# Kernel tuning notes

Hardware: AMD Instinct MI355X
Metric: run time of the kernel (lower is better)

The kernel has to match this reference:

```python
import jax, jax.numpy as jnp
import numpy as np

HEADS = 8
DIM_HEAD = 64
SCALE = DIM_HEAD ** -0.5
LN_EPS = 1e-5
NEG_INF = -1e30


def layernorm(x, gamma, beta):
    mu = jnp.mean(x, axis=-1, keepdims=True)
    var = jnp.var(x, axis=-1, keepdims=True)
    return (x - mu) * jax.lax.rsqrt(var + LN_EPS) * gamma + beta


def setup_inputs() -> dict:
    key = jax.random.key(0)
    ks = jax.random.split(key, 8)
    b, f, n, d, inner = 8, 8192, 64, 1024, HEADS * DIM_HEAD
    x = jax.random.normal(ks[0], (b, f, d), dtype=jnp.float32)
    latents = jax.random.normal(ks[1], (b, n, d), dtype=jnp.float32)
    key_padding_mask = jax.random.randint(ks[2], (b, f), 0, 2) > 0  # True = padded
    s = 0.02
    return {
        "x": x,
        "latents": latents,
        "key_padding_mask": key_padding_mask,
        "kv_gate": jnp.float32(-4.0),
        "gamma_media": jnp.ones((d,), jnp.float32),
        "beta_media": jnp.zeros((d,), jnp.float32),
        "gamma_lat": jnp.ones((d,), jnp.float32),
        "beta_lat": jnp.zeros((d,), jnp.float32),
        "Wq": jax.random.normal(ks[3], (d, inner), jnp.float32) * s,
        "Wk": jax.random.normal(ks[4], (d, inner), jnp.float32) * s,
        "Wv": jax.random.normal(ks[5], (d, inner), jnp.float32) * s,
        "Wout": jax.random.normal(ks[6], (inner, d), jnp.float32) * s,
    }


def reference(x, latents, key_padding_mask, kv_gate, gamma_media, beta_media,
              gamma_lat, beta_lat, Wq, Wk, Wv, Wout):
    b, f, d = x.shape
    n = latents.shape[1]
    x = layernorm(x, gamma_media, beta_media)
    latents = layernorm(latents, gamma_lat, beta_lat)
    kv = jnp.concatenate((x, latents * kv_gate), axis=1)  # (b, f+n, d)

    q = (latents @ Wq).reshape(b, n, HEADS, DIM_HEAD)       # (b, q, h, d)
    k = (kv @ Wk).reshape(b, f + n, HEADS, DIM_HEAD)        # (b, kv, h, d)
    v = (kv @ Wv).reshape(b, f + n, HEADS, DIM_HEAD)

    sim = jnp.einsum('bqhd,bkhd->bhqk', q * SCALE, k)       # (b, h, n, f+n)
    sim = sim - jax.lax.stop_gradient(jnp.max(sim, axis=-1, keepdims=True))

    valid_feat = ~key_padding_mask                          # (b, f)
    valid_full = jnp.concatenate(
        (valid_feat, jnp.ones((b, n), dtype=bool)), axis=1)  # (b, f+n)
    sim = jnp.where(valid_full[:, None, None, :], sim, NEG_INF)

    attn = jax.nn.softmax(sim, axis=-1)
    out = jnp.einsum('bhqk,bkhd->bqhd', attn, v).reshape(b, n, HEADS * DIM_HEAD)
    return out @ Wout
```

## Files before the change

### kernel.cpp

```cpp
#include <hip/hip_runtime.h>
#include <stdint.h>


#define KVPAD 8448
#define NCHUNK 17

typedef __attribute__((ext_vector_type(8))) short short8;
typedef __attribute__((ext_vector_type(4))) float f32x4;

typedef __attribute__((address_space(1))) void gvoid;
typedef __attribute__((address_space(3))) void lvoid;

__device__ __forceinline__ unsigned short f2bf(float f) {
    union { float f; uint32_t u; } v; v.f = f;
    uint32_t u = v.u;
    u += 0x7fffu + ((u >> 16) & 1u);
    return (unsigned short)(u >> 16);
}

__device__ __forceinline__ void mfma16(f32x4& c, short8 a, short8 b) {
    asm volatile("v_mfma_f32_16x16x32_bf16 %0, %1, %2, %0"
                 : "+v"(c) : "v"(a), "v"(b));
}

__device__ __forceinline__ void gl2lds16(const void* g, void* l) {
    __builtin_amdgcn_global_load_lds((gvoid*)g, (lvoid*)l, 16, 0, 0);
}

__device__ __forceinline__ void pbar() {
    asm volatile("" ::: "memory");
    __builtin_amdgcn_s_barrier();
    asm volatile("" ::: "memory");
}
#define WAITVM(N) asm volatile("s_waitcnt vmcnt(" #N ")" ::: "memory")

__global__ __launch_bounds__(1024) void scan_kernel(
    const int* __restrict__ mask, int* __restrict__ pfx, int* __restrict__ cnt)
{
    __shared__ int wsum[16];
    int b = blockIdx.x;
    int t = threadIdx.x, lane = t & 63, w = t >> 6;
    int c[8], tot = 0;
#pragma unroll
    for (int k = 0; k < 8; k++) {
        c[k] = (mask[b * 8192 + k * 1024 + t] == 0) ? 1 : 0;
        tot += c[k];
    }
    int run = tot;
#pragma unroll
    for (int off = 1; off < 64; off <<= 1) {
        int u = __shfl_up(run, off);
        if (lane >= off) run += u;
    }
    if (lane == 63) wsum[w] = run;
    __syncthreads();
    if (t < 16) {
        int v = wsum[t];
#pragma unroll
        for (int off = 1; off < 16; off <<= 1) {
            int u = __shfl_up(v, off);
            if (t >= off) v += u;
        }
        wsum[t] = v;
        if (t == 15) cnt[b] = v;
    }
    __syncthreads();
    int base = (w ? wsum[w - 1] : 0) + (run - tot);
#pragma unroll
    for (int k = 0; k < 8; k++) {
        pfx[b * 8192 + k * 1024 + t] = base;
        base += c[k];
    }
}

__global__ __launch_bounds__(256) void prep_kernel(
    const float* __restrict__ X, const float* __restrict__ latents,
    const int* __restrict__ mask, const int* __restrict__ pfx,
    const float* __restrict__ gm, const float* __restrict__ bm,
    const float* __restrict__ gl, const float* __restrict__ bl,
    const float* __restrict__ Wk, const float* __restrict__ Wv,
    const float* __restrict__ Wq, const float* __restrict__ Wout,
    unsigned short* __restrict__ x_ln, unsigned short* __restrict__ lat_ln,
    unsigned short* __restrict__ WkvqT, unsigned short* __restrict__ WoutT)
{
    __shared__ float t[64][65];
    int blk = blockIdx.x;
    if (blk >= 16512) {
        int tt = blk - 16512;
        int z = tt >> 7, u = tt & 127;
        const float* S; unsigned short* D; int R, C, bx, by;
        if (z == 0)      { S = Wk;   D = WkvqT;                       R = 1024; C = 512;  by = u >> 3; bx = u & 7; }
        else if (z == 1) { S = Wv;   D = WkvqT + (size_t)512 * 1024;  R = 1024; C = 512;  by = u >> 3; bx = u & 7; }
        else if (z == 2) { S = Wq;   D = WkvqT + (size_t)1024 * 1024; R = 1024; C = 512;  by = u >> 3; bx = u & 7; }
        else             { S = Wout; D = WoutT;                       R = 512;  C = 1024; by = u >> 4; bx = u & 15; }
        int r0 = by * 64, c0 = bx * 64;
#pragma unroll
        for (int i = 0; i < 16; i++) {
            int o = i * 256 + threadIdx.x;
            int rr = o >> 6, cc = o & 63;
            t[rr][cc] = S[(size_t)(r0 + rr) * C + c0 + cc];
        }
        __syncthreads();
#pragma unroll
        for (int i = 0; i < 16; i++) {
            int o = i * 256 + threadIdx.x;
            int cl = o >> 6, rl = o & 63;
            D[(size_t)(c0 + cl) * R + r0 + rl] = f2bf(t[rl][cl]);
        }
        return;
    }
    int lane = threadIdx.x & 63;
    int row = blk * 4 + (threadIdx.x >> 6);
    const float *src, *g, *bet;
    unsigned short* dst;
    if (row < 65536) {
        if (mask[row] != 0) return;
        int b = row >> 13;
        src = X + (size_t)row * 1024;
        dst = x_ln + ((size_t)b * 8192 + pfx[row]) * 1024;
        g = gm; bet = bm;
    } else {
        int r = row - 65536;
        src = latents + (size_t)r * 1024;
        dst = lat_ln + (size_t)r * 1024;
        g = gl; bet = bl;
    }
    const float4* xr = (const float4*)src;
    float4 v[4];
    float s = 0.f, s2 = 0.f;
#pragma unroll
    for (int i = 0; i < 4; i++) {
        v[i] = xr[i * 64 + lane];
        s  += v[i].x + v[i].y + v[i].z + v[i].w;
        s2 += v[i].x*v[i].x + v[i].y*v[i].y + v[i].z*v[i].z + v[i].w*v[i].w;
    }
#pragma unroll
    for (int off = 1; off < 64; off <<= 1) {
        s += __shfl_xor(s, off);
        s2 += __shfl_xor(s2, off);
    }
    float mean = s * (1.0f / 1024.0f);
    float var  = s2 * (1.0f / 1024.0f) - mean * mean;
    float rs = rsqrtf(var + 1e-5f);
    ushort4* yr = (ushort4*)dst;
    const float4* gp = (const float4*)g;
    const float4* bp = (const float4*)bet;
#pragma unroll
    for (int i = 0; i < 4; i++) {
        int c4 = i * 64 + lane;
        float4 gg = gp[c4], bb = bp[c4];
        ushort4 o;
        o.x = f2bf((v[i].x - mean) * rs * gg.x + bb.x);
        o.y = f2bf((v[i].y - mean) * rs * gg.y + bb.y);
        o.z = f2bf((v[i].z - mean) * rs * gg.z + bb.z);
        o.w = f2bf((v[i].w - mean) * rs * gg.w + bb.w);
        yr[c4] = o;
    }
}

__global__ __launch_bounds__(512, 2) void gemm256(
    const unsigned short* __restrict__ A,
    const unsigned short* __restrict__ BT,
    unsigned short* __restrict__ Ck,
    unsigned short* __restrict__ CvT,
    const int* __restrict__ cnt)
{
    __shared__ unsigned short lds[65536];
    int bx = blockIdx.x, by = blockIdx.y;
    int lid = by * 4 + bx;
    lid = (lid & 7) * 128 + (lid >> 3);
    bx = lid & 3; by = lid >> 2;
    int rowbase = by * 256;
    int colbase = bx * 256;
    int bq = by >> 5;
    int rl0 = (by & 31) * 256;
    if (rl0 >= cnt[bq]) return;

    int tid = threadIdx.x;
    int lane = tid & 63;
    int wid = tid >> 6;
    int qd = lane >> 4, cc = lane & 15;
    int wm = wid >> 2, wn = wid & 3;

    f32x4 acc[8][4];
#pragma unroll
    for (int mf = 0; mf < 8; mf++)
#pragma unroll
        for (int nf = 0; nf < 4; nf++)
            acc[mf][nf] = (f32x4){0.f, 0.f, 0.f, 0.f};

#define STAGE_TILE(buf, kt)                                                     \
    {                                                                           \
        int bb = (buf) * 32768;                                                 \
        _Pragma("unroll")                                                       \
        for (int i = 0; i < 4; i++) {                                           \
            int s = i * 512 + tid;                                              \
            int m = s >> 3, kc = s & 7;                                         \
            int kg = kc ^ (m & 7);                                              \
            gl2lds16(A + (size_t)(rowbase + m) * 1024 + (kt) * 64 + kg * 8,     \
                     &lds[bb + s * 8]);                                         \
        }                                                                       \
        _Pragma("unroll")                                                       \
        for (int i = 0; i < 4; i++) {                                           \
            int s = i * 512 + tid;                                              \
            int m = s >> 3, kc = s & 7;                                         \
            int kg = kc ^ (m & 7);                                              \
            gl2lds16(BT + (size_t)(colbase + m) * 1024 + (kt) * 64 + kg * 8,    \
                     &lds[bb + 16384 + s * 8]);                                 \
        }                                                                       \
    }

    STAGE_TILE(0, 0);
    WAITVM(0);
    pbar();

    int cur = 0;
#pragma unroll 1
    for (int kt = 0; kt < 16; kt++) {
        bool pf = (kt < 15);
        int ab = cur * 32768;
        int bb = ab + 16384;
        short8 bf0[4], bf1[4], af[4];

        if (pf) STAGE_TILE(cur ^ 1, kt + 1);
#pragma unroll
        for (int nf = 0; nf < 4; nf++) {
            int n = wn * 64 + nf * 16 + cc;
            bf0[nf] = *(const short8*)&lds[bb + (n * 8 + (qd ^ (n & 7))) * 8];
        }
#pragma unroll
        for (int i = 0; i < 4; i++) {
            int m = wm * 128 + i * 16 + cc;
            af[i] = *(const short8*)&lds[ab + (m * 8 + (qd ^ (m & 7))) * 8];
        }
        __builtin_amdgcn_s_setprio(1);
#pragma unroll
        for (int i = 0; i < 4; i++)
#pragma unroll
            for (int nf = 0; nf < 4; nf++)
                mfma16(acc[i][nf], af[i], bf0[nf]);
        __builtin_amdgcn_s_setprio(0);
        pbar();

#pragma unroll
        for (int i = 0; i < 4; i++) {
            int m = wm * 128 + (4 + i) * 16 + cc;
            af[i] = *(const short8*)&lds[ab + (m * 8 + (qd ^ (m & 7))) * 8];
        }
        __builtin_amdgcn_s_setprio(1);
#pragma unroll
        for (int i = 0; i < 4; i++)
#pragma unroll
            for (int nf = 0; nf < 4; nf++)
                mfma16(acc[4 + i][nf], af[i], bf0[nf]);
        __builtin_amdgcn_s_setprio(0);
        pbar();

#pragma unroll
        for (int nf = 0; nf < 4; nf++) {
            int n = wn * 64 + nf * 16 + cc;
            bf1[nf] = *(const short8*)&lds[bb + (n * 8 + ((4 + qd) ^ (n & 7))) * 8];
        }
#pragma unroll
        for (int i = 0; i < 4; i++) {
            int m = wm * 128 + i * 16 + cc;
            af[i] = *(const short8*)&lds[ab + (m * 8 + ((4 + qd) ^ (m & 7))) * 8];
        }
        __builtin_amdgcn_s_setprio(1);
#pragma unroll
        for (int i = 0; i < 4; i++)
#pragma unroll
            for (int nf = 0; nf < 4; nf++)
                mfma16(acc[i][nf], af[i], bf1[nf]);
        __builtin_amdgcn_s_setprio(0);
        pbar();

#pragma unroll
        for (int i = 0; i < 4; i++) {
            int m = wm * 128 + (4 + i) * 16 + cc;
            af[i] = *(const short8*)&lds[ab + (m * 8 + ((4 + qd) ^ (m & 7))) * 8];
        }
        __builtin_amdgcn_s_setprio(1);
#pragma unroll
        for (int i = 0; i < 4; i++)
#pragma unroll
            for (int nf = 0; nf < 4; nf++)
                mfma16(acc[4 + i][nf], af[i], bf1[nf]);
        __builtin_amdgcn_s_setprio(0);
        if (pf) WAITVM(0);
        pbar();
        cur ^= 1;
    }
#undef STAGE_TILE

    bool isK = (colbase < 512);
#pragma unroll
    for (int mf = 0; mf < 8; mf++) {
        int grow = rl0 + wm * 128 + mf * 16 + qd * 4;
#pragma unroll
        for (int nf = 0; nf < 4; nf++) {
            int col = colbase + wn * 64 + nf * 16 + cc;
            if (isK) {
#pragma unroll
                for (int r = 0; r < 4; r++)
                    Ck[(size_t)(bq * KVPAD + 64 + grow + r) * 512 + col] =
                        f2bf(acc[mf][nf][r]);
            } else {
                ushort4 pk;
                pk.x = f2bf(acc[mf][nf][0]);
                pk.y = f2bf(acc[mf][nf][1]);
                pk.z = f2bf(acc[mf][nf][2]);
                pk.w = f2bf(acc[mf][nf][3]);
                *(ushort4*)&CvT[((size_t)bq * 512 + (col - 512)) * KVPAD + 64 + grow] = pk;
            }
        }
    }
}

__global__ __launch_bounds__(256) void gemm_bf16(
    const unsigned short* __restrict__ A, const unsigned short* __restrict__ BT,
    int Kd,
    unsigned short* __restrict__ Ck, float* __restrict__ Cf,
    unsigned short* __restrict__ CvT, unsigned short* __restrict__ Qb,
    int nsplit, int nq, int ldc, int P, int Sstride, int Ofs,
    float scale_const, float qscale, const float* __restrict__ scale_ptr,
    const int* __restrict__ cnt)
{
    __shared__ unsigned short a_lds[128 * 64];
    __shared__ unsigned short b_lds[128 * 64];
    int bx = blockIdx.x, by = blockIdx.y;
    size_t rowbase = (size_t)by * 128;
    size_t colbase = (size_t)bx * 128;
    if (cnt) {
        int bq = (int)rowbase / P, rl = (int)rowbase - bq * P;
        if (rl >= cnt[bq]) return;
    }
    int tid = threadIdx.x;
    int lane = tid & 63;
    int wave = tid >> 6;
    int wrow = (wave >> 1) * 64, wcol = (wave & 1) * 64;
    int qd = lane >> 4, cc = lane & 15;

    f32x4 acc[4][4];
#pragma unroll
    for (int mt = 0; mt < 4; mt++)
#pragma unroll
        for (int nt = 0; nt < 4; nt++)
            acc[mt][nt] = (f32x4){0.f, 0.f, 0.f, 0.f};

    int kiters = Kd >> 6;
    for (int kt = 0; kt < kiters; kt++) {
        int k0 = kt << 6;
#pragma unroll
        for (int i = 0; i < 4; i++) {
            int s = i * 256 + tid;
            int m = s >> 3, kc = s & 7;
            int kg = kc ^ (m & 7);
            gl2lds16(A + (rowbase + m) * (size_t)Kd + (k0 + kg * 8), &a_lds[s * 8]);
        }
#pragma unroll
        for (int i = 0; i < 4; i++) {
            int s = i * 256 + tid;
            int m = s >> 3, kc = s & 7;
            int kg = kc ^ (m & 7);
            gl2lds16(BT + (colbase + m) * (size_t)Kd + (k0 + kg * 8), &b_lds[s * 8]);
        }
        __syncthreads();
#pragma unroll
        for (int ks = 0; ks < 2; ks++) {
            short8 af[4], bfr[4];
            int cg = ks * 4 + qd;
#pragma unroll
            for (int mt = 0; mt < 4; mt++) {
                int m = wrow + mt * 16 + cc;
                af[mt] = *(const short8*)&a_lds[(m * 8 + (cg ^ (m & 7))) * 8];
            }
#pragma unroll
            for (int nt = 0; nt < 4; nt++) {
                int n = wcol + nt * 16 + cc;
                bfr[nt] = *(const short8*)&b_lds[(n * 8 + (cg ^ (n & 7))) * 8];
            }
#pragma unroll
            for (int mt = 0; mt < 4; mt++)
#pragma unroll
                for (int nt = 0; nt < 4; nt++)
                    mfma16(acc[mt][nt], af[mt], bfr[nt]);
        }
        __syncthreads();
    }

    float sc = scale_const;
    if (scale_ptr) sc *= *scale_ptr;
#pragma unroll
    for (int mt = 0; mt < 4; mt++) {
        int g0 = (int)rowbase + wrow + mt * 16 + qd * 4;
        int bq = g0 / P, rl = g0 - bq * P;
#pragma unroll
        for (int nt = 0; nt < 4; nt++) {
            int col = (int)colbase + wcol + nt * 16 + cc;
            if (col >= nq) {
#pragma unroll
                for (int r = 0; r < 4; r++)
                    Qb[(size_t)(bq * 64 + rl + r) * 512 + (col - nq)] =
                        f2bf(acc[mt][nt][r] * qscale);
            } else if (col < nsplit) {
                int idx0 = bq * Sstride + Ofs + rl;
                if (Cf) {
#pragma unroll
                    for (int r = 0; r < 4; r++)
                        Cf[(size_t)(idx0 + r) * ldc + col] = acc[mt][nt][r] * sc;
                } else {
#pragma unroll
                    for (int r = 0; r < 4; r++)
                        Ck[(size_t)(idx0 + r) * ldc + col] = f2bf(acc[mt][nt][r] * sc);
                }
            } else {
                ushort4 pk;
                pk.x = f2bf(acc[mt][nt][0] * sc);
                pk.y = f2bf(acc[mt][nt][1] * sc);
                pk.z = f2bf(acc[mt][nt][2] * sc);
                pk.w = f2bf(acc[mt][nt][3] * sc);
                *(ushort4*)&CvT[((size_t)bq * 512 + (col - nsplit)) * KVPAD + Ofs + rl] = pk;
            }
        }
    }
}

__global__ __launch_bounds__(256) void attn_kernel(
    const unsigned short* __restrict__ Kbuf,
    const unsigned short* __restrict__ Vt,
    const unsigned short* __restrict__ Qbuf,
    const int* __restrict__ cnt,
    float* __restrict__ Opart,
    float* __restrict__ Mpart,
    float* __restrict__ Lpart)
{
    __shared__ unsigned short P_lds[64 * 264];
    __shared__ float red_max[4][64];
    __shared__ float red_sum[4][64];
    __shared__ float mrow[64];
    __shared__ float lrow[64];
    __shared__ float frow[64];

    int chunk = blockIdx.x, h = blockIdx.y, b = blockIdx.z;
    int len = 64 + cnt[b];
    int kv0 = chunk * 512;
    if (kv0 >= len) return;

    int tid = threadIdx.x, lane = tid & 63, w = tid >> 6;
    int qd = lane >> 4, cc = lane & 15;
    int pidx = (b * 8 + h) * NCHUNK + chunk;

    short8 qf[4][2];
    const unsigned short* Qb = Qbuf + ((size_t)b * 64) * 512 + h * 64;
#pragma unroll
    for (int mt = 0; mt < 4; mt++)
#pragma unroll
        for (int ks = 0; ks < 2; ks++)
            qf[mt][ks] = *(const short8*)&Qb[(size_t)(mt * 16 + cc) * 512 + ks * 32 + qd * 8];

    f32x4 acco[4];
#pragma unroll
    for (int mt = 0; mt < 4; mt++) acco[mt] = (f32x4){0.f, 0.f, 0.f, 0.f};

    const unsigned short* Kb = Kbuf + (size_t)b * KVPAD * 512 + h * 64;
    const unsigned short* Vbase = Vt + ((size_t)b * 512 + h * 64 + w * 16 + cc) * KVPAD;

#pragma unroll 1
    for (int s = 0; s < 2; s++) {
        int kvs = kv0 + s * 256;
        if (kvs >= len) break;
        int kvw = kvs + w * 64;

        f32x4 acc[4][4];
#pragma unroll
        for (int mt = 0; mt < 4; mt++)
#pragma unroll
            for (int nt = 0; nt < 4; nt++)
                acc[mt][nt] = (f32x4){0.f, 0.f, 0.f, 0.f};
#pragma unroll
        for (int nt = 0; nt < 4; nt++) {
            int kvr = kvw + nt * 16 + cc;
#pragma unroll
            for (int ks = 0; ks < 2; ks++) {
                short8 kf = *(const short8*)&Kb[(size_t)kvr * 512 + ks * 32 + qd * 8];
#pragma unroll
                for (int mt = 0; mt < 4; mt++)
                    mfma16(acc[mt][nt], qf[mt][ks], kf);
            }
        }
#pragma unroll
        for (int nt = 0; nt < 4; nt++) {
            int kv = kvw + nt * 16 + cc;
            if (kv >= len) {
#pragma unroll
                for (int mt = 0; mt < 4; mt++)
#pragma unroll
                    for (int r = 0; r < 4; r++) acc[mt][nt][r] = -1e30f;
            }
        }
        float vmax[4][4];
#pragma unroll
        for (int mt = 0; mt < 4; mt++)
#pragma unroll
            for (int r = 0; r < 4; r++)
                vmax[mt][r] = fmaxf(fmaxf(acc[mt][0][r], acc[mt][1][r]),
                                    fmaxf(acc[mt][2][r], acc[mt][3][r]));
#pragma unroll
        for (int off = 1; off < 16; off <<= 1)
#pragma unroll
            for (int mt = 0; mt < 4; mt++)
#pragma unroll
                for (int r = 0; r < 4; r++)
                    vmax[mt][r] = fmaxf(vmax[mt][r], __shfl_xor(vmax[mt][r], off));
        if (cc == 0) {
#pragma unroll
            for (int mt = 0; mt < 4; mt++)
#pragma unroll
                for (int r = 0; r < 4; r++)
                    red_max[w][mt * 16 + qd * 4 + r] = vmax[mt][r];
        }
        __syncthreads();
        if (tid < 64) {
            float tmax = fmaxf(fmaxf(red_max[0][tid], red_max[1][tid]),
                               fmaxf(red_max[2][tid], red_max[3][tid]));
            if (s == 0) {
                mrow[tid] = tmax;
            } else {
                float mo = mrow[tid];
                float mn = fmaxf(mo, tmax);
                frow[tid] = __expf(mo - mn);
                mrow[tid] = mn;
            }
        }
        __syncthreads();
        float vsum[4][4];
#pragma unroll
        for (int mt = 0; mt < 4; mt++)
#pragma unroll
            for (int r = 0; r < 4; r++) {
                int row = mt * 16 + qd * 4 + r;
                float m = mrow[row];
                float ssum = 0.f;
#pragma unroll
                for (int nt = 0; nt < 4; nt++) {
                    float p = __expf(acc[mt][nt][r] - m);
                    ssum += p;
                    P_lds[row * 264 + w * 64 + nt * 16 + cc] = f2bf(p);
                }
                vsum[mt][r] = ssum;
            }
#pragma unroll
        for (int off = 1; off < 16; off <<= 1)
#pragma unroll
            for (int mt = 0; mt < 4; mt++)
#pragma unroll
                for (int r = 0; r < 4; r++)
                    vsum[mt][r] += __shfl_xor(vsum[mt][r], off);
        if (cc == 0) {
#pragma unroll
            for (int mt = 0; mt < 4; mt++)
#pragma unroll
                for (int r = 0; r < 4; r++)
                    red_sum[w][mt * 16 + qd * 4 + r] = vsum[mt][r];
        }
        __syncthreads();
        if (tid < 64) {
            float snew = red_sum[0][tid] + red_sum[1][tid] +
                         red_sum[2][tid] + red_sum[3][tid];
            lrow[tid] = (s == 0) ? snew : lrow[tid] * frow[tid] + snew;
        }
        if (s > 0) {
#pragma unroll
            for (int mt = 0; mt < 4; mt++)
#pragma unroll
                for (int r = 0; r < 4; r++)
                    acco[mt][r] *= frow[mt * 16 + qd * 4 + r];
        }
        const unsigned short* Vb = Vbase + kvs;
#pragma unroll
        for (int ks = 0; ks < 8; ks++) {
            short8 vf = *(const short8*)&Vb[ks * 32 + qd * 8];
#pragma unroll
            for (int mt = 0; mt < 4; mt++) {
                short8 pf = *(const short8*)&P_lds[(size_t)(mt * 16 + cc) * 264 + ks * 32 + qd * 8];
                mfma16(acco[mt], pf, vf);
            }
        }
    }

    if (tid < 64) {
        Mpart[(size_t)pidx * 64 + tid] = mrow[tid];
        Lpart[(size_t)pidx * 64 + tid] = lrow[tid];
    }
    float* Ob = Opart + (size_t)pidx * 4096;
#pragma unroll
    for (int mt = 0; mt < 4; mt++)
#pragma unroll
        for (int r = 0; r < 4; r++)
            Ob[(size_t)(mt * 16 + qd * 4 + r) * 64 + w * 16 + cc] = acco[mt][r];
}

__global__ __launch_bounds__(256) void combine_kernel(
    const float* __restrict__ Opart, const float* __restrict__ Mpart,
    const float* __restrict__ Lpart, const int* __restrict__ cnt,
    unsigned short* __restrict__ AttnOut)
{
    __shared__ float wls[NCHUNK][16];
    __shared__ float invl[16];
    int bh = blockIdx.x >> 2, qg = blockIdx.x & 3;
    int b = bh >> 3, h = bh & 7;
    int pbase = bh * NCHUNK;
    int nact = (64 + cnt[b] + 511) >> 9;
    int tid = threadIdx.x;
    if (tid < 16) {
        int q = qg * 16 + tid;
        float M = -3.0e38f;
        for (int cn = 0; cn < nact; cn++)
            M = fmaxf(M, Mpart[(size_t)(pbase + cn) * 64 + q]);
        float l = 0.f;
        for (int cn = 0; cn < nact; cn++) {
            float wc = __expf(Mpart[(size_t)(pbase + cn) * 64 + q] - M);
            wls[cn][tid] = wc;
            l += wc * Lpart[(size_t)(pbase + cn) * 64 + q];
        }
        invl[tid] = 1.0f / l;
    }
    __syncthreads();
    int ql = tid >> 4, d4 = (tid & 15) * 4;
    int q = qg * 16 + ql;
    float ax = 0.f, ay = 0.f, az = 0.f, aw = 0.f;
    for (int cn = 0; cn < nact; cn++) {
        float wc = wls[cn][ql];
        float4 o = *(const float4*)&Opart[((size_t)(pbase + cn) * 64 + q) * 64 + d4];
        ax += wc * o.x; ay += wc * o.y; az += wc * o.z; aw += wc * o.w;
    }
    float iv = invl[ql];
    ushort4 pk;
    pk.x = f2bf(ax * iv); pk.y = f2bf(ay * iv);
    pk.z = f2bf(az * iv); pk.w = f2bf(aw * iv);
    *(ushort4*)&AttnOut[((size_t)b * 64 + q) * 512 + h * 64 + d4] = pk;
}

#define OPART_OFF    ((size_t)0)
#define MPART_OFF    ((size_t)34603008)
#define LPART_OFF    ((size_t)35143680)
#define XLN_OFF      ((size_t)0)
#define LATLN_OFF    ((size_t)134217728)
#define KBUF_OFF     ((size_t)135266304)
#define VT_OFF       ((size_t)204472320)
#define WKVQT_OFF    ((size_t)273678336)
#define WOUTT_OFF    ((size_t)276824064)
#define PFX_OFF      ((size_t)277872640)
#define CNT_OFF      ((size_t)278134784)
#define QBUF_OFF     ((size_t)278134912)
#define ATTNOUT_OFF  ((size_t)278659200)

extern "C" void kernel_launch(void* const* d_in, const int* in_sizes, int n_in,
                              void* d_out, int out_size, void* d_ws, size_t ws_size,
                              hipStream_t stream) {
    const float* x       = (const float*)d_in[0];
    const float* latents = (const float*)d_in[1];
    const int*   mask    = (const int*)d_in[2];
    const float* kv_gate = (const float*)d_in[3];
    const float* gm      = (const float*)d_in[4];
    const float* bm      = (const float*)d_in[5];
    const float* gl      = (const float*)d_in[6];
    const float* bl      = (const float*)d_in[7];
    const float* Wq      = (const float*)d_in[8];
    const float* Wk      = (const float*)d_in[9];
    const float* Wv      = (const float*)d_in[10];
    const float* Wout    = (const float*)d_in[11];
    float* out = (float*)d_out;

    char* ws = (char*)d_ws;
    float* Opart = (float*)(ws + OPART_OFF);
    float* Mpart = (float*)(ws + MPART_OFF);
    float* Lpart = (float*)(ws + LPART_OFF);
    unsigned short* Qbuf    = (unsigned short*)(ws + QBUF_OFF);
    unsigned short* AttnOut = (unsigned short*)(ws + ATTNOUT_OFF);
    unsigned short* x_ln    = (unsigned short*)(ws + XLN_OFF);
    unsigned short* lat_ln  = (unsigned short*)(ws + LATLN_OFF);
    unsigned short* Kbuf    = (unsigned short*)(ws + KBUF_OFF);
    unsigned short* Vt      = (unsigned short*)(ws + VT_OFF);
    unsigned short* WkvqT   = (unsigned short*)(ws + WKVQT_OFF);
    unsigned short* WoutT   = (unsigned short*)(ws + WOUTT_OFF);
    int* pfx = (int*)(ws + PFX_OFF);
    int* cnt = (int*)(ws + CNT_OFF);

    scan_kernel<<<8, 1024, 0, stream>>>(mask, pfx, cnt);

    prep_kernel<<<17024, 256, 0, stream>>>(
        x, latents, mask, pfx, gm, bm, gl, bl, Wk, Wv, Wq, Wout,
        x_ln, lat_ln, WkvqT, WoutT);

    gemm_bf16<<<dim3(12, 4), 256, 0, stream>>>(
        lat_ln, WkvqT, 1024, Kbuf, nullptr, Vt, Qbuf,
        512, 1024, 512, 64, KVPAD, 0, 1.0f, 0.125f, kv_gate, nullptr);

    gemm256<<<dim3(4, 256), 512, 0, stream>>>(x_ln, WkvqT, Kbuf, Vt, cnt);

    attn_kernel<<<dim3(NCHUNK, 8, 8), 256, 0, stream>>>(
        Kbuf, Vt, Qbuf, cnt, Opart, Mpart, Lpart);

    combine_kernel<<<256, 256, 0, stream>>>(Opart, Mpart, Lpart, cnt, AttnOut);

    gemm_bf16<<<dim3(8, 4), 256, 0, stream>>>(
        AttnOut, WoutT, 512, nullptr, out, nullptr, nullptr,
        1 << 30, 1 << 30, 1024, 64, 64, 0, 1.0f, 0.f, nullptr, nullptr);
}
```

Measured before the change: 539.3 us.

## Interleave half-tile global-to-LDS staging with MFMA phases in KV projection GEMM

Restructures the K/V projection GEMM main loop into a finer-grained software pipeline. Tiles are now staged in half-tile pieces, interleaved between MFMA sub-blocks, and B tiles are prefetched one step further ahead, with partial vmcnt waits replacing full drains. Each MFMA phase now covers both k-halves per fragment load instead of one. The aim is to hide global load latency and remove the full-wait bubble at each k-tile. In exchange it adds more barriers and more register pressure, and the intricate buffer-parity ordering is a correctness risk.

Result: no change. 534.9 us (-0.8%).

```diff
diff --git a/kernel.cpp b/kernel.cpp
--- a/kernel.cpp
+++ b/kernel.cpp
@@ -189,109 +189,113 @@
         for (int nf = 0; nf < 4; nf++)
             acc[mf][nf] = (f32x4){0.f, 0.f, 0.f, 0.f};
 
-#define STAGE_TILE(buf, kt)                                                     \
-    {                                                                           \
-        int bb = (buf) * 32768;                                                 \
-        _Pragma("unroll")                                                       \
-        for (int i = 0; i < 4; i++) {                                           \
-            int s = i * 512 + tid;                                              \
-            int m = s >> 3, kc = s & 7;                                         \
-            int kg = kc ^ (m & 7);                                              \
-            gl2lds16(A + (size_t)(rowbase + m) * 1024 + (kt) * 64 + kg * 8,     \
-                     &lds[bb + s * 8]);                                         \
-        }                                                                       \
-        _Pragma("unroll")                                                       \
-        for (int i = 0; i < 4; i++) {                                           \
-            int s = i * 512 + tid;                                              \
-            int m = s >> 3, kc = s & 7;                                         \
-            int kg = kc ^ (m & 7);                                              \
-            gl2lds16(BT + (size_t)(colbase + m) * 1024 + (kt) * 64 + kg * 8,    \
-                     &lds[bb + 16384 + s * 8]);                                 \
-        }                                                                       \
-    }
-
-    STAGE_TILE(0, 0);
-    WAITVM(0);
+#define STAGE_HALF(par, isB, h, kt)                                            \
+    if ((kt) < 16) {                                                           \
+        const unsigned short* srcb = (isB) ? BT : A;                           \
+        int rb = (isB) ? colbase : rowbase;                                    \
+        _Pragma("unroll")                                                      \
+        for (int i = 0; i < 2; i++) {                                          \
+            int s = i * 512 + tid;                                             \
+            int ml = s >> 3, kc = s & 7;                                       \
+            int kg = kc ^ (ml & 7);                                            \
+            gl2lds16(srcb + (size_t)(rb + (h) * 128 + ml) * 1024               \
+                          + (kt) * 64 + kg * 8,                                \
+                     &lds[(par) * 32768 + (isB) * 16384 + (h) * 8192 + s * 8]);\
+        }                                                                      \
+    }
+
+#define RD_A(par, mh)                                                          \
+    _Pragma("unroll")                                                          \
+    for (int i = 0; i < 4; i++) {                                              \
+        int m = wm * 128 + ((mh) * 4 + i) * 16 + cc;                           \
+        _Pragma("unroll")                                                      \
+        for (int ks = 0; ks < 2; ks++) {                                       \
+            int cg = ks * 4 + qd;                                              \
+            afr[i][ks] = *(const short8*)&lds[(par) * 32768 +                  \
+                              (m * 8 + (cg ^ (m & 7))) * 8];                   \
+        }                                                                      \
+    }
+
+#define RD_B(par, nfp, dst)                                                    \
+    _Pragma("unroll")                                                          \
+    for (int j = 0; j < 2; j++) {                                              \
+        int n = wn * 64 + ((nfp) * 2 + j) * 16 + cc;                           \
+        _Pragma("unroll")                                                      \
+        for (int ks = 0; ks < 2; ks++) {                                       \
+            int cg = ks * 4 + qd;                                              \
+            dst[j][ks] = *(const short8*)&lds[(par) * 32768 + 16384 +          \
+                              (n * 8 + (cg ^ (n & 7))) * 8];                   \
+        }                                                                      \
+    }
+
+#define DO_MFMA(mh, nfp, bsrc)                                                 \
+    __builtin_amdgcn_s_setprio(1);                                             \
+    _Pragma("unroll")                                                          \
+    for (int i = 0; i < 4; i++)                                                \
+        _Pragma("unroll")                                                      \
+        for (int j = 0; j < 2; j++)                                            \
+            _Pragma("unroll")                                                  \
+            for (int ks = 0; ks < 2; ks++)                                     \
+                mfma16(acc[(mh) * 4 + i][(nfp) * 2 + j],                       \
+                       afr[i][ks], bsrc[j][ks]);                               \
+    __builtin_amdgcn_s_setprio(0);
+
+    STAGE_HALF(0, 0, 0, 0); STAGE_HALF(0, 0, 1, 0);
+    STAGE_HALF(0, 1, 0, 0); STAGE_HALF(0, 1, 1, 0);
+    STAGE_HALF(1, 1, 0, 1); STAGE_HALF(1, 1, 1, 1);
+    WAITVM(4);
     pbar();
 
-    int cur = 0;
+    short8 afr[4][2], bfr0[2][2], bfr1[2][2];
 #pragma unroll 1
-    for (int kt = 0; kt < 16; kt++) {
-        bool pf = (kt < 15);
-        int ab = cur * 32768;
-        int bb = ab + 16384;
-        short8 bf0[4], bf1[4], af[4];
-
-        if (pf) STAGE_TILE(cur ^ 1, kt + 1);
-#pragma unroll
-        for (int nf = 0; nf < 4; nf++) {
-            int n = wn * 64 + nf * 16 + cc;
-            bf0[nf] = *(const short8*)&lds[bb + (n * 8 + (qd ^ (n & 7))) * 8];
-        }
-#pragma unroll
-        for (int i = 0; i < 4; i++) {
-            int m = wm * 128 + i * 16 + cc;
-            af[i] = *(const short8*)&lds[ab + (m * 8 + (qd ^ (m & 7))) * 8];
-        }
-        __builtin_amdgcn_s_setprio(1);
-#pragma unroll
-        for (int i = 0; i < 4; i++)
-#pragma unroll
-            for (int nf = 0; nf < 4; nf++)
-                mfma16(acc[i][nf], af[i], bf0[nf]);
-        __builtin_amdgcn_s_setprio(0);
-        pbar();
-
-#pragma unroll
-        for (int i = 0; i < 4; i++) {
-            int m = wm * 128 + (4 + i) * 16 + cc;
-            af[i] = *(const short8*)&lds[ab + (m * 8 + (qd ^ (m & 7))) * 8];
-        }
-        __builtin_amdgcn_s_setprio(1);
-#pragma unroll
-        for (int i = 0; i < 4; i++)
-#pragma unroll
-            for (int nf = 0; nf < 4; nf++)
-                mfma16(acc[4 + i][nf], af[i], bf0[nf]);
-        __builtin_amdgcn_s_setprio(0);
-        pbar();
-
-#pragma unroll
-        for (int nf = 0; nf < 4; nf++) {
-            int n = wn * 64 + nf * 16 + cc;
-            bf1[nf] = *(const short8*)&lds[bb + (n * 8 + ((4 + qd) ^ (n & 7))) * 8];
-        }
-#pragma unroll
-        for (int i = 0; i < 4; i++) {
-            int m = wm * 128 + i * 16 + cc;
-            af[i] = *(const short8*)&lds[ab + (m * 8 + ((4 + qd) ^ (m & 7))) * 8];
-        }
-        __builtin_amdgcn_s_setprio(1);
-#pragma unroll
-        for (int i = 0; i < 4; i++)
-#pragma unroll
-            for (int nf = 0; nf < 4; nf++)
-                mfma16(acc[i][nf], af[i], bf1[nf]);
-        __builtin_amdgcn_s_setprio(0);
-        pbar();
-
-#pragma unroll
-        for (int i = 0; i < 4; i++) {
-            int m = wm * 128 + (4 + i) * 16 + cc;
-            af[i] = *(const short8*)&lds[ab + (m * 8 + ((4 + qd) ^ (m & 7))) * 8];
-        }
-        __builtin_amdgcn_s_setprio(1);
-#pragma unroll
-        for (int i = 0; i < 4; i++)
-#pragma unroll
-            for (int nf = 0; nf < 4; nf++)
-                mfma16(acc[4 + i][nf], af[i], bf1[nf]);
-        __builtin_amdgcn_s_setprio(0);
-        if (pf) WAITVM(0);
-        pbar();
-        cur ^= 1;
-    }
-#undef STAGE_TILE
+    for (int it = 0; it < 8; it++) {
+        int t1k = 2 * it + 1, t2k = 2 * it + 2, t3k = 2 * it + 3;
+
+        RD_A(0, 0); RD_B(0, 0, bfr0);
+        STAGE_HALF(1, 0, 0, t1k);
+        pbar();
+        DO_MFMA(0, 0, bfr0);
+        pbar();
+        RD_B(0, 1, bfr1);
+        STAGE_HALF(1, 0, 1, t1k);
+        pbar();
+        DO_MFMA(0, 1, bfr1);
+        pbar();
+        RD_A(0, 1);
+        STAGE_HALF(0, 1, 0, t2k);
+        pbar();
+        DO_MFMA(1, 0, bfr0);
+        pbar();
+        STAGE_HALF(0, 1, 1, t2k);
+        pbar();
+        DO_MFMA(1, 1, bfr1);
+        if (it < 7) { WAITVM(4); } else { WAITVM(0); }
+        pbar();
+        RD_A(1, 0); RD_B(1, 0, bfr0);
+        STAGE_HALF(0, 0, 0, t2k);
+        pbar();
+        DO_MFMA(0, 0, bfr0);
+        pbar();
+        RD_B(1, 1, bfr1);
+        STAGE_HALF(0, 0, 1, t2k);
+        pbar();
+        DO_MFMA(0, 1, bfr1);
+        pbar();
+        RD_A(1, 1);
+        STAGE_HALF(1, 1, 0, t3k);
+        pbar();
+        DO_MFMA(1, 0, bfr0);
+        pbar();
+        STAGE_HALF(1, 1, 1, t3k);
+        pbar();
+        DO_MFMA(1, 1, bfr1);
+        WAITVM(4);
+        pbar();
+    }
+#undef STAGE_HALF
+#undef RD_A
+#undef RD_B
+#undef DO_MFMA
 
     bool isK = (colbase < 512);
 #pragma unroll
```
